# Kernel optimization log

Measured on AMD Instinct MI355X. Metric: run time of the kernel, lower is better.

The kernel has to match this reference:

```python
import jax, jax.numpy as jnp
import numpy as np


def _segsum(x):
    """Stable segment-sum. x: (..., l) -> (..., l, l) lower-triangular sums."""
    l = x.shape[-1]
    cs = jnp.cumsum(x, axis=-1)
    seg = cs[..., :, None] - cs[..., None, :]
    mask = jnp.tril(jnp.ones((l, l), dtype=bool))
    return jnp.where(mask, seg, -jnp.inf)


def setup_inputs() -> dict:
    key = jax.random.key(0)
    kx, ka, kb, kc = jax.random.split(key, 4)
    b, s, h, p, n = 4, 8192, 32, 64, 16
    X = jax.random.normal(kx, (b, s, h, p), dtype=jnp.float32)
    # negative A for realistic decaying SSM dynamics / numerical safety
    A = -jnp.abs(jax.random.normal(ka, (b, s, h), dtype=jnp.float32)) * 0.5
    B = jax.random.normal(kb, (b, s, h, n), dtype=jnp.float32)
    C = jax.random.normal(kc, (b, s, h, n), dtype=jnp.float32)
    return {"X": X, "A": A, "B": B, "C": C, "block_len": 64}


def reference(X, A, B, C, block_len):
    b, s, h, p = X.shape
    n = B.shape[-1]
    c = s // block_len
    l = block_len
    # chunk: (b, c, l, ...)
    Xb = X.reshape(b, c, l, h, p)
    Bb = B.reshape(b, c, l, h, n)
    Cb = C.reshape(b, c, l, h, n)
    Ab = A.reshape(b, c, l, h).transpose(0, 3, 1, 2)  # (b, h, c, l)
    A_cumsum = jnp.cumsum(Ab, axis=-1)                # (b, h, c, l)

    # 1) intra-chunk (diagonal) output
    L = jnp.exp(_segsum(Ab))                          # (b, h, c, l, l)
    Y_diag = jnp.einsum("bclhn,bcshn,bhcls,bcshp->bclhp", Cb, Bb, L, Xb)

    # 2) intra-chunk states (chunk-final state contribution)
    decay_states = jnp.exp(A_cumsum[..., -1:] - A_cumsum)   # (b, h, c, l)
    states = jnp.einsum("bclhn,bhcl,bclhp->bchpn", Bb, decay_states, Xb)

    # 3) inter-chunk recurrence (zero initial states)
    A_last = A_cumsum[..., -1]                        # (b, h, c)
    decay_chunk = jnp.exp(_segsum(jnp.pad(A_last, ((0, 0), (0, 0), (1, 0)))))  # (b,h,c+1,c+1)
    states = jnp.concatenate([jnp.zeros_like(states[:, :1]), states], axis=1)  # (b,c+1,h,p,n)
    new_states = jnp.einsum("bhzc,bchpn->bzhpn", decay_chunk, states)
    states = new_states[:, :-1]                       # states entering each chunk

    # 4) state -> output (off-diagonal)
    state_decay_out = jnp.exp(A_cumsum)               # (b, h, c, l)
    Y_off = jnp.einsum("bclhn,bchpn,bhcl->bclhp", Cb, states, state_decay_out)

    Y = (Y_diag + Y_off).reshape(b, s, h, p)
    return Y
```

## Files before the change

### kernel.cpp

```cpp
#include <hip/hip_runtime.h>

#define BB 4
#define SS 8192
#define HH 32
#define PP 64
#define NN 16
#define LL 64
#define CC 128
#define NCHAIN (BB * HH)
#define NCHT (NCHAIN * CC)
#define ITERS 8
#define GRID1 (NCHT / ITERS)

typedef __attribute__((ext_vector_type(8))) short bf16x8;
typedef __attribute__((ext_vector_type(4))) short s16x4;
typedef __attribute__((ext_vector_type(4))) float f32x4;

#define LBAR() do { \
    __builtin_amdgcn_sched_barrier(0); \
    asm volatile("s_waitcnt lgkmcnt(0)" ::: "memory"); \
    __builtin_amdgcn_s_barrier(); \
    __builtin_amdgcn_sched_barrier(0); \
} while (0)

__device__ inline short f2bf(float f) {
    unsigned u = __builtin_bit_cast(unsigned, f);
    u = (u + 0x7FFFu + ((u >> 16) & 1u)) >> 16;
    return (short)u;
}
__device__ inline float bf2f(short s) {
    unsigned u = ((unsigned)(unsigned short)s) << 16;
    return __builtin_bit_cast(float, u);
}
__device__ inline float wscan(float v, int l) {
    float x = v;
#pragma unroll
    for (int d = 1; d < 64; d <<= 1) {
        float t = __shfl_up(x, d, 64);
        if (l >= d) x += t;
    }
    return x;
}

__global__ __launch_bounds__(256) void k1_states(
    const float* __restrict__ X, const float* __restrict__ A,
    const float* __restrict__ B, short* __restrict__ states,
    float* __restrict__ alast_g, short* __restrict__ xtf, int do_xtf)
{
    int tid = threadIdx.x;
    int w = tid >> 6, l = tid & 63, g = l >> 4, lr = l & 15;
    int r = tid >> 2, q4 = tid & 3;
    int bid = blockIdx.x;

    __shared__ float Bs[2][LL][17];

    float xrA[16], xrB[16];
    float4 br; float av;

#define K1_LOADS(gc_, xr_) { \
    int h_ = (gc_) & 31, c_ = ((gc_) >> 5) & 127, b_ = (gc_) >> 12; \
    size_t row0_ = (size_t)b_ * SS + (size_t)c_ * LL; \
    const float* Xp_ = X + (row0_ * HH + h_) * PP; \
    av = (A + row0_ * HH + h_)[(size_t)l * HH]; \
    br = *(const float4*)(B + (row0_ * HH + h_) * NN + (size_t)r * (HH * NN) + q4 * 4); \
    _Pragma("unroll") for (int kt_ = 0; kt_ < 2; ++kt_) \
    _Pragma("unroll") for (int e_ = 0; e_ < 8; ++e_) \
        xr_[kt_ * 8 + e_] = Xp_[(size_t)(kt_ * 32 + g * 8 + e_) * (HH * PP) + 16 * w + lr]; }

#define K1_STAGE(qd_, gc_) { \
    float x_ = wscan(av, l); \
    float alast_ = __shfl(x_, 63, 64); \
    float wlr_ = __expf(alast_ - __shfl(x_, r, 64)); \
    Bs[qd_][r][q4 * 4 + 0] = br.x * wlr_; \
    Bs[qd_][r][q4 * 4 + 1] = br.y * wlr_; \
    Bs[qd_][r][q4 * 4 + 2] = br.z * wlr_; \
    Bs[qd_][r][q4 * 4 + 3] = br.w * wlr_; \
    if (tid == 0) { \
        int h_ = (gc_) & 31, c_ = ((gc_) >> 5) & 127, b_ = (gc_) >> 12; \
        alast_g[(b_ * HH + h_) * CC + c_] = alast_; } }

#define K1_COMPUTE(qd_, xr_, gc_) { \
    int h_ = (gc_) & 31, c_ = ((gc_) >> 5) & 127, b_ = (gc_) >> 12; \
    size_t cc_ = (size_t)((b_ * HH + h_) * CC + c_); \
    bf16x8 bt0_, bt1_, xf0_, xf1_; \
    _Pragma("unroll") for (int e_ = 0; e_ < 8; ++e_) { \
        bt0_[e_] = f2bf(Bs[qd_][g * 8 + e_][lr]); \
        bt1_[e_] = f2bf(Bs[qd_][32 + g * 8 + e_][lr]); \
        xf0_[e_] = f2bf(xr_[e_]); xf1_[e_] = f2bf(xr_[8 + e_]); } \
    f32x4 st_ = __builtin_amdgcn_mfma_f32_16x16x32_bf16(bt0_, xf0_, (f32x4)0.f, 0, 0, 0); \
    st_ = __builtin_amdgcn_mfma_f32_16x16x32_bf16(bt1_, xf1_, st_, 0, 0, 0); \
    s16x4 sp_ = { f2bf(st_[0]), f2bf(st_[1]), f2bf(st_[2]), f2bf(st_[3]) }; \
    *(s16x4*)(states + (cc_ << 10) + ((16 * w + lr) << 4) + (g << 2)) = sp_; \
    if (do_xtf) { \
        short* xd_ = xtf + (cc_ << 12); \
        ((bf16x8*)xd_)[tid] = xf0_; \
        ((bf16x8*)xd_)[tid + 256] = xf1_; } }

    K1_LOADS(bid, xrA)
    K1_STAGE(0, bid)
    LBAR();
#pragma unroll
    for (int t = 0; t < ITERS; ++t) {
        int gc_c = bid + t * GRID1;
        int gc_n = bid + (t + 1) * GRID1;
        if (t + 1 < ITERS) {
            if (t & 1) { K1_LOADS(gc_n, xrA) } else { K1_LOADS(gc_n, xrB) }
        }
        if (t & 1) { K1_COMPUTE(t & 1, xrB, gc_c) } else { K1_COMPUTE(t & 1, xrA, gc_c) }
        if (t + 1 < ITERS) {
            K1_STAGE((t & 1) ^ 1, gc_n)
            LBAR();
        }
    }
#undef K1_LOADS
#undef K1_STAGE
#undef K1_COMPUTE
}

__global__ __launch_bounds__(256) void k2_scan(
    short* __restrict__ states, const float* __restrict__ alast_g)
{
    int chain = blockIdx.x >> 1;
    int t2 = ((blockIdx.x & 1) << 8) + threadIdx.x;
    __shared__ float eal[CC];
    if (threadIdx.x < CC)
        eal[threadIdx.x] = __expf(alast_g[chain * CC + threadIdx.x]);
    __syncthreads();

    unsigned* base = (unsigned*)(states + ((size_t)chain * CC << 10)) + t2;
    float P0 = 0.f, P1 = 0.f;
    for (int c0 = 0; c0 < CC; c0 += 8) {
        unsigned s[8];
#pragma unroll
        for (int u = 0; u < 8; ++u) s[u] = base[(size_t)(c0 + u) << 9];
#pragma unroll
        for (int u = 0; u < 8; ++u) {
            float e = eal[c0 + u];
            float f0 = bf2f((short)(s[u] & 0xFFFFu));
            float f1 = bf2f((short)(s[u] >> 16));
            unsigned o = (unsigned)(unsigned short)f2bf(P0)
                       | ((unsigned)(unsigned short)f2bf(P1) << 16);
            P0 = e * P0 + f0;
            P1 = e * P1 + f1;
            base[(size_t)(c0 + u) << 9] = o;
        }
    }
}

__global__ __launch_bounds__(256) void k3_big(
    const float* __restrict__ A, const float* __restrict__ Bm,
    const float* __restrict__ Cm, const short* __restrict__ pin,
    const short* __restrict__ xtf, float* __restrict__ Y)
{
    int tid = threadIdx.x;
    int w = tid >> 6, l = tid & 63, g = l >> 4, lr = l & 15;
    int r = tid >> 2, q4 = tid & 3;
    int bid = blockIdx.x;

    __shared__ short ScF[8 * 64 * 8];
    __shared__ short BsF[4 * 64 * 8];
    __shared__ short CsF[4 * 64 * 8];
    __shared__ short PF [4 * 64 * 8];

    ((bf16x8*)ScF)[tid] = (bf16x8)0;
    ((bf16x8*)ScF)[tid + 256] = (bf16x8)0;
    if (tid < 128) {
        int zs = (tid >> 5) * 64 + 32 + (tid & 31);
        ((bf16x8*)BsF)[zs] = (bf16x8)0;
        ((bf16x8*)CsF)[zs] = (bf16x8)0;
        ((bf16x8*)PF )[zs] = (bf16x8)0;
    }

    bf16x8 xv0n, xv1n, xv0c, xv1c;
    float4 br, crv;
    s16x4 pinb; float av;
    float x_c, x_n;

#define K3_LOADS(gc_) { \
    int h_ = (gc_) & 31, c_ = ((gc_) >> 5) & 127, b_ = (gc_) >> 12; \
    size_t row0_ = (size_t)b_ * SS + (size_t)c_ * LL; \
    size_t cc_ = (size_t)((b_ * HH + h_) * CC + c_); \
    const short* xs_ = xtf + (cc_ << 12); \
    xv0n = ((const bf16x8*)xs_)[tid]; \
    xv1n = ((const bf16x8*)xs_)[tid + 256]; \
    av = (A + row0_ * HH + h_)[(size_t)l * HH]; \
    br = *(const float4*)(Bm + (row0_ * HH + h_) * NN + (size_t)r * (HH * NN) + q4 * 4); \
    crv = *(const float4*)(Cm + (row0_ * HH + h_) * NN + (size_t)r * (HH * NN) + q4 * 4); \
    pinb = *(const s16x4*)(pin + (cc_ << 10) + ((16 * w + lr) << 4) + (g << 2)); }

#define K3_STAGE() { \
    x_n = wscan(av, l); \
    int fl_ = (r & 15) + 16 * (q4 >> 1); \
    int jt_ = r >> 4; \
    s16x4 bb_ = { f2bf(br.x), f2bf(br.y), f2bf(br.z), f2bf(br.w) }; \
    ((s16x4*)BsF)[(jt_ * 64 + fl_) * 2 + (q4 & 1)] = bb_; \
    s16x4 cc_ = { f2bf(crv.x), f2bf(crv.y), f2bf(crv.z), f2bf(crv.w) }; \
    ((s16x4*)CsF)[(jt_ * 64 + fl_) * 2 + (q4 & 1)] = cc_; \
    ((s16x4*)PF)[(w * 64 + (g >> 1) * 16 + lr) * 2 + (g & 1)] = pinb; }

#define SCORE_TILE(IT, JT, MASK) { \
    bf16x8 ca_ = ((bf16x8*)CsF)[(IT) * 64 + l]; \
    bf16x8 bw_ = ((bf16x8*)BsF)[(JT) * 64 + l]; \
    f32x4 sr_ = __builtin_amdgcn_mfma_f32_16x16x32_bf16(ca_, bw_, (f32x4)0.f, 0, 0, 0); \
    float enj_ = __shfl(en_l, (JT) * 16 + lr, 64); \
    _Pragma("unroll") for (int rr = 0; rr < 4; ++rr) { \
        float v_ = sr_[rr] * (__shfl(ei_l, 16 * (IT) + 4 * g + rr, 64) * enj_); \
        if (MASK) v_ = ((JT) * 16 + lr <= (IT) * 16 + 4 * g + rr) ? v_ : 0.f; \
        ScF[(((IT) * 2 + ((JT) >> 1)) * 64 + ((2 * (JT) + (lr >> 3)) & 3) * 16 + 4 * g + rr) * 8 + (lr & 7)] = f2bf(v_); } }

    K3_LOADS(bid)
    K3_STAGE()
    x_c = x_n; xv0c = xv0n; xv1c = xv1n;
    LBAR();

#pragma unroll 2
    for (int t = 0; t < ITERS; ++t) {
        int gc = bid + t * GRID1;
        if (t + 1 < ITERS) { K3_LOADS(bid + (t + 1) * GRID1) }

        float ei_l = __expf(x_c);
        float en_l = __expf(-x_c);

        __builtin_amdgcn_s_setprio(1);
        f32x4 acc[4];
        {
            bf16x8 pfw = ((bf16x8*)PF)[w * 64 + l];
#pragma unroll
            for (int it = 0; it < 4; ++it) {
                bf16x8 ca = ((bf16x8*)CsF)[it * 64 + l];
                acc[it] = __builtin_amdgcn_mfma_f32_16x16x32_bf16(ca, pfw, (f32x4)0.f, 0, 0, 0);
            }
#pragma unroll
            for (int it = 0; it < 4; ++it)
#pragma unroll
                for (int rr = 0; rr < 4; ++rr)
                    acc[it][rr] *= __shfl(ei_l, 16 * it + 4 * g + rr, 64);
        }

        if (w == 0)      { SCORE_TILE(0,0,true)  SCORE_TILE(2,1,false) SCORE_TILE(3,2,false) }
        else if (w == 1) { SCORE_TILE(1,0,false) SCORE_TILE(2,2,true)  SCORE_TILE(3,3,true)  }
        else if (w == 2) { SCORE_TILE(1,1,true)  SCORE_TILE(3,0,false) }
        else             { SCORE_TILE(2,0,false) SCORE_TILE(3,1,false) }
        __builtin_amdgcn_s_setprio(0);

        LBAR();

        __builtin_amdgcn_s_setprio(1);
#pragma unroll
        for (int it = 0; it < 4; ++it) {
            bf16x8 af0 = ((bf16x8*)ScF)[(it * 2 + 0) * 64 + l];
            acc[it] = __builtin_amdgcn_mfma_f32_16x16x32_bf16(af0, xv0c, acc[it], 0, 0, 0);
        }
#pragma unroll
        for (int it = 2; it < 4; ++it) {
            bf16x8 af1 = ((bf16x8*)ScF)[(it * 2 + 1) * 64 + l];
            acc[it] = __builtin_amdgcn_mfma_f32_16x16x32_bf16(af1, xv1c, acc[it], 0, 0, 0);
        }
        __builtin_amdgcn_s_setprio(0);
        {
            int h_ = gc & 31, c_ = (gc >> 5) & 127, b_ = gc >> 12;
            size_t row0_ = (size_t)b_ * SS + (size_t)c_ * LL;
            float* Yp = Y + (row0_ * HH + h_) * PP;
#pragma unroll
            for (int it = 0; it < 4; ++it)
#pragma unroll
                for (int rr = 0; rr < 4; ++rr)
                    Yp[(size_t)(16 * it + 4 * g + rr) * (HH * PP) + 16 * w + lr] = acc[it][rr];
        }

        if (t + 1 < ITERS) { K3_STAGE() }
        LBAR();
        x_c = x_n; xv0c = xv0n; xv1c = xv1n;
    }
#undef K3_LOADS
#undef K3_STAGE
#undef SCORE_TILE
}

__global__ __launch_bounds__(256) void k3_small(
    const float* __restrict__ X, const float* __restrict__ A,
    const float* __restrict__ Bm, const float* __restrict__ Cm,
    const short* __restrict__ pin, float* __restrict__ Y)
{
    int blk = blockIdx.x;
    int h = blk & (HH - 1);
    int c = (blk >> 5) & (CC - 1);
    int b = blk >> 12;
    int tid = threadIdx.x;
    int w = tid >> 6, l = tid & 63, g = l >> 4, lr = l & 15;
    int chain = b * HH + h;
    int r = tid >> 2, q = tid & 3;

    __shared__ short XTF[8 * 64 * 8];
    __shared__ short ScF[8 * 64 * 8];
    __shared__ short BsF[4 * 64 * 8];
    __shared__ short PF[4 * 64 * 8];

    size_t row0 = (size_t)b * SS + (size_t)c * LL;
    const float* Xp = X + (row0 * HH + h) * PP;
    const float* Bp = Bm + (row0 * HH + h) * NN;
    const float* Cp = Cm + (row0 * HH + h) * NN;
    const float* Ap = A + row0 * HH + h;
    float* Yp = Y + (row0 * HH + h) * PP;

    float av = Ap[(size_t)l * HH];
    float4 br = *(const float4*)(Bp + (size_t)r * (HH * NN) + q * 4);
    float4 cr0 = {0,0,0,0}, cr1 = {0,0,0,0};
    if (g < 2) {
        const float* crp = Cp + (size_t)(16 * w + lr) * (HH * NN) + g * 8;
        cr0 = *(const float4*)crp;
        cr1 = *(const float4*)(crp + 4);
    }
    s16x4 pinb = *(const s16x4*)(pin + (((size_t)(chain * CC + c)) << 10) + ((16 * w + lr) << 4) + (g << 2));
    float xr[16];
#pragma unroll
    for (int si = 0; si < 2; ++si)
#pragma unroll
        for (int e = 0; e < 8; ++e)
            xr[si * 8 + e] = Xp[(size_t)(si * 32 + g * 8 + e) * (HH * PP) + 16 * w + lr];

    float x = wscan(av, l);

    ((bf16x8*)ScF)[w * 128 + l] = (bf16x8)0;
    ((bf16x8*)ScF)[w * 128 + 64 + l] = (bf16x8)0;
    if (tid < 128)
        ((bf16x8*)PF)[(tid >> 5) * 64 + 32 + (tid & 31)] = (bf16x8)0;
    {
        int zt = tid >> 6, zu = (tid >> 1) & 31, zv = tid & 1;
        ((s16x4*)BsF)[(zt * 64 + 32 + zu) * 2 + zv] = (s16x4)0;
    }
    {
        int fl = (r & 15) + 16 * (q >> 1);
        int jt = r >> 4;
        s16x4 bb = { f2bf(br.x), f2bf(br.y), f2bf(br.z), f2bf(br.w) };
        ((s16x4*)BsF)[(jt * 64 + fl) * 2 + (q & 1)] = bb;
    }
    *(s16x4*)&PF[(w * 64 + (g >> 1) * 16 + lr) * 8 + (g & 1) * 4] = pinb;
    bf16x8 caw = (bf16x8)0;
    if (g < 2) {
        caw[0] = f2bf(cr0.x); caw[1] = f2bf(cr0.y);
        caw[2] = f2bf(cr0.z); caw[3] = f2bf(cr0.w);
        caw[4] = f2bf(cr1.x); caw[5] = f2bf(cr1.y);
        caw[6] = f2bf(cr1.z); caw[7] = f2bf(cr1.w);
    }
    __syncthreads();

    float cs_i[4], ei[4];
    int ib = 16 * w + 4 * g;
#pragma unroll
    for (int rr = 0; rr < 4; ++rr) {
        cs_i[rr] = __shfl(x, ib + rr, 64);
        ei[rr] = __expf(cs_i[rr]);
    }

    f32x4 acc[4];
#pragma unroll
    for (int pt = 0; pt < 4; ++pt) {
        bf16x8 pfv = ((bf16x8*)PF)[pt * 64 + l];
        acc[pt] = __builtin_amdgcn_mfma_f32_16x16x32_bf16(caw, pfv, (f32x4)0.f, 0, 0, 0);
    }
#pragma unroll
    for (int pt = 0; pt < 4; ++pt)
#pragma unroll
        for (int rr = 0; rr < 4; ++rr) acc[pt][rr] *= ei[rr];

    for (int jt = 0; jt <= w; ++jt) {
        bf16x8 bw = ((bf16x8*)BsF)[jt * 64 + l];
        f32x4 sr = __builtin_amdgcn_mfma_f32_16x16x32_bf16(caw, bw, (f32x4)0.f, 0, 0, 0);
        int j = jt * 16 + lr;
        float csj = __shfl(x, j, 64);
        int kt2 = j >> 5;
        int flb = 16 * ((j >> 3) & 3);
#pragma unroll
        for (int rr = 0; rr < 4; ++rr) {
            int i15 = g * 4 + rr;
            int i = 16 * w + i15;
            float v = (j <= i) ? sr[rr] * __expf(cs_i[rr] - csj) : 0.f;
            ScF[((w * 2 + kt2) * 64 + i15 + flb) * 8 + (j & 7)] = f2bf(v);
        }
    }

#pragma unroll
    for (int si = 0; si < 2; ++si) {
        bf16x8 xb;
#pragma unroll
        for (int e = 0; e < 8; ++e) xb[e] = f2bf(xr[si * 8 + e]);
        ((bf16x8*)XTF)[tid + si * 256] = xb;
    }
    __syncthreads();

    int kts = (w >= 2) ? 2 : 1;
    for (int kt = 0; kt < kts; ++kt) {
        bf16x8 af = ((bf16x8*)ScF)[(w * 2 + kt) * 64 + l];
#pragma unroll
        for (int pt = 0; pt < 4; ++pt) {
            bf16x8 xf = ((bf16x8*)XTF)[(kt * 4 + pt) * 64 + l];
            acc[pt] = __builtin_amdgcn_mfma_f32_16x16x32_bf16(af, xf, acc[pt], 0, 0, 0);
        }
    }

#pragma unroll
    for (int pt = 0; pt < 4; ++pt)
#pragma unroll
        for (int rr = 0; rr < 4; ++rr)
            Yp[(size_t)(16 * w + 4 * g + rr) * (HH * PP) + pt * 16 + lr] = acc[pt][rr];
}

extern "C" void kernel_launch(void* const* d_in, const int* in_sizes, int n_in,
                              void* d_out, int out_size, void* d_ws, size_t ws_size,
                              hipStream_t stream)
{
    const float* X = (const float*)d_in[0];
    const float* A = (const float*)d_in[1];
    const float* B = (const float*)d_in[2];
    const float* C = (const float*)d_in[3];
    float* Y = (float*)d_out;

    const size_t states_bytes = (size_t)NCHT * 1024 * 2;
    const size_t alast_bytes  = (size_t)NCHT * 4;
    const size_t xtf_bytes    = (size_t)NCHT * 4096 * 2;
    short* states = (short*)d_ws;
    float* alast  = (float*)((char*)d_ws + states_bytes);
    short* xtf    = (short*)((char*)d_ws + states_bytes + alast_bytes);
    int big = (ws_size >= states_bytes + alast_bytes + xtf_bytes) ? 1 : 0;

    dim3 blk(256);
    k1_states<<<dim3(GRID1), blk, 0, stream>>>(X, A, B, states, alast, xtf, big);
    k2_scan<<<dim3(NCHAIN * 2), blk, 0, stream>>>(states, alast);
    if (big)
        k3_big<<<dim3(GRID1), blk, 0, stream>>>(A, B, C, states, xtf, Y);
    else
        k3_small<<<dim3(NCHT), blk, 0, stream>>>(X, A, B, C, states, Y);
}
```

Measured before the change: 251.8 us.

## Swizzle score LDS layout and load X operands late to cut register pressure

The score tile written to shared memory now uses an XOR swizzle on the row index, and the MFMA reads apply the same swizzle, to reduce LDS bank conflicts. X fragment loads for the next chunk are no longer prefetched at the top of the iteration into extra registers. They are issued after the Y stores and before staging, which removes the double-buffered X registers. This lowers VGPR use but exposes more of the X load latency before the next iteration's MFMAs.

```diff
diff --git a/kernel.cpp b/kernel.cpp
--- a/kernel.cpp
+++ b/kernel.cpp
@@ -155,6 +155,7 @@
     int tid = threadIdx.x;
     int w = tid >> 6, l = tid & 63, g = l >> 4, lr = l & 15;
     int r = tid >> 2, q4 = tid & 3;
+    int lsw = l ^ ((l >> 2) & 3);
     int bid = blockIdx.x;
 
     __shared__ short ScF[8 * 64 * 8];
@@ -171,22 +172,26 @@
         ((bf16x8*)PF )[zs] = (bf16x8)0;
     }
 
-    bf16x8 xv0n, xv1n, xv0c, xv1c;
+    bf16x8 xv0c, xv1c;
     float4 br, crv;
     s16x4 pinb; float av;
     float x_c, x_n;
 
-#define K3_LOADS(gc_) { \
+#define K3_LOADS_SC(gc_) { \
     int h_ = (gc_) & 31, c_ = ((gc_) >> 5) & 127, b_ = (gc_) >> 12; \
     size_t row0_ = (size_t)b_ * SS + (size_t)c_ * LL; \
     size_t cc_ = (size_t)((b_ * HH + h_) * CC + c_); \
-    const short* xs_ = xtf + (cc_ << 12); \
-    xv0n = ((const bf16x8*)xs_)[tid]; \
-    xv1n = ((const bf16x8*)xs_)[tid + 256]; \
     av = (A + row0_ * HH + h_)[(size_t)l * HH]; \
     br = *(const float4*)(Bm + (row0_ * HH + h_) * NN + (size_t)r * (HH * NN) + q4 * 4); \
     crv = *(const float4*)(Cm + (row0_ * HH + h_) * NN + (size_t)r * (HH * NN) + q4 * 4); \
     pinb = *(const s16x4*)(pin + (cc_ << 10) + ((16 * w + lr) << 4) + (g << 2)); }
+
+#define K3_LOADS_X(gc_) { \
+    int h_ = (gc_) & 31, c_ = ((gc_) >> 5) & 127, b_ = (gc_) >> 12; \
+    size_t cc_ = (size_t)((b_ * HH + h_) * CC + c_); \
+    const short* xs_ = xtf + (cc_ << 12); \
+    xv0c = ((const bf16x8*)xs_)[tid]; \
+    xv1c = ((const bf16x8*)xs_)[tid + 256]; }
 
 #define K3_STAGE() { \
     x_n = wscan(av, l); \
@@ -206,17 +211,20 @@
     _Pragma("unroll") for (int rr = 0; rr < 4; ++rr) { \
         float v_ = sr_[rr] * (__shfl(ei_l, 16 * (IT) + 4 * g + rr, 64) * enj_); \
         if (MASK) v_ = ((JT) * 16 + lr <= (IT) * 16 + 4 * g + rr) ? v_ : 0.f; \
-        ScF[(((IT) * 2 + ((JT) >> 1)) * 64 + ((2 * (JT) + (lr >> 3)) & 3) * 16 + 4 * g + rr) * 8 + (lr & 7)] = f2bf(v_); } }
-
-    K3_LOADS(bid)
+        int idx_ = ((2 * (JT) + (lr >> 3)) & 3) * 16 + 4 * g + rr; \
+        int sw_ = idx_ ^ ((idx_ >> 2) & 3); \
+        ScF[(((IT) * 2 + ((JT) >> 1)) * 64 + sw_) * 8 + (lr & 7)] = f2bf(v_); } }
+
+    K3_LOADS_SC(bid)
+    K3_LOADS_X(bid)
     K3_STAGE()
-    x_c = x_n; xv0c = xv0n; xv1c = xv1n;
+    x_c = x_n;
     LBAR();
 
 #pragma unroll 2
     for (int t = 0; t < ITERS; ++t) {
         int gc = bid + t * GRID1;
-        if (t + 1 < ITERS) { K3_LOADS(bid + (t + 1) * GRID1) }
+        if (t + 1 < ITERS) { K3_LOADS_SC(bid + (t + 1) * GRID1) }
 
         float ei_l = __expf(x_c);
         float en_l = __expf(-x_c);
@@ -248,12 +256,12 @@
         __builtin_amdgcn_s_setprio(1);
 #pragma unroll
         for (int it = 0; it < 4; ++it) {
-            bf16x8 af0 = ((bf16x8*)ScF)[(it * 2 + 0) * 64 + l];
+            bf16x8 af0 = ((bf16x8*)ScF)[(it * 2 + 0) * 64 + lsw];
             acc[it] = __builtin_amdgcn_mfma_f32_16x16x32_bf16(af0, xv0c, acc[it], 0, 0, 0);
         }
 #pragma unroll
         for (int it = 2; it < 4; ++it) {
-            bf16x8 af1 = ((bf16x8*)ScF)[(it * 2 + 1) * 64 + l];
+            bf16x8 af1 = ((bf16x8*)ScF)[(it * 2 + 1) * 64 + lsw];
             acc[it] = __builtin_amdgcn_mfma_f32_16x16x32_bf16(af1, xv1c, acc[it], 0, 0, 0);
         }
         __builtin_amdgcn_s_setprio(0);
@@ -268,11 +276,15 @@
                     Yp[(size_t)(16 * it + 4 * g + rr) * (HH * PP) + 16 * w + lr] = acc[it][rr];
         }
 
-        if (t + 1 < ITERS) { K3_STAGE() }
+        if (t + 1 < ITERS) {
+            K3_LOADS_X(bid + (t + 1) * GRID1)
+            K3_STAGE()
+        }
         LBAR();
-        x_c = x_n; xv0c = xv0n; xv1c = xv1n;
-    }
-#undef K3_LOADS
+        x_c = x_n;
+    }
+#undef K3_LOADS_SC
+#undef K3_LOADS_X
 #undef K3_STAGE
 #undef SCORE_TILE
 }
```

Result: no change. 251.2 us (-0.2%).
